# Kernel optimization log

Hardware: AMD Instinct MI355X
Metric: run time of the kernel (lower is better)

## Reference

```python
import jax, jax.numpy as jnp
import numpy as np

N_STEPS = 64          # sample['N']
G = 1.0               # sample['g'] (constant diffusion)
NUM_SAMPLES = 2       # num_samples_per_obs
W_SCALE = 0.05

# interpolant coefficients: alpha(s)=1-s, beta(s)=s, sigma(s)=1-s
# derivatives: alpha_dot=-1, beta_dot=1, sigma_dot=-1

def b_net(x, x0, s, W1, b1, W2, b2, W3, b3):
    # B_net(interpolant, current_state, s): MLP on concat([x, x0, s])
    sf = jnp.full(x.shape[:-1] + (1,), s, dtype=x.dtype)
    inp = jnp.concatenate([x, x0, sf], axis=-1)      # [B, 2*dim+1]
    h = jax.nn.relu(inp @ W1 + b1)
    h = jax.nn.relu(h @ W2 + b2)
    return h @ W3 + b3                                # [B, dim]


def setup_inputs() -> dict:
    key = jax.random.key(0)
    ks = jax.random.split(key, 4)
    num_obs, dim, hid = 65536, 64, 256
    X0 = jax.random.normal(ks[0], (num_obs, dim), dtype=jnp.float32)
    W1 = jax.random.normal(ks[1], (2 * dim + 1, hid), dtype=jnp.float32) * W_SCALE
    W2 = jax.random.normal(ks[2], (hid, hid), dtype=jnp.float32) * W_SCALE
    W3 = jax.random.normal(ks[3], (hid, dim), dtype=jnp.float32) * W_SCALE
    return {
        "X0": X0,
        "W1": W1, "b1": jnp.zeros((hid,), jnp.float32),
        "W2": W2, "b2": jnp.zeros((hid,), jnp.float32),
        "W3": W3, "b3": jnp.zeros((dim,), jnp.float32),
    }


def reference(X0, W1, b1, W2, b2, W3, b3):
    time = jnp.linspace(0.0, 1.0, N_STEPS + 1, dtype=X0.dtype)
    ds = jnp.asarray(1.0 / N_STEPS, X0.dtype)
    sqrt_ds = jnp.sqrt(ds)
    params = (W1, b1, W2, b2, W3, b3)

    def sample_one(key):
        k0, kloop = jax.random.split(key)
        # first Euler step: X = X0 + ds*B(X0,X0,0) + sigma(0)*sqrt(ds)*eta
        eta0 = jax.random.normal(k0, X0.shape, X0.dtype)
        X = X0 + ds * b_net(X0, X0, time[0], *params) + (1.0 - time[0]) * sqrt_ds * eta0

        def step(carry, n):
            X, key = carry
            key, kn = jax.random.split(key)
            s = time[n]
            al, ald = 1.0 - s, -1.0
            bt, btd = s, 1.0
            sg, sgd = 1.0 - s, -1.0
            drift_b = b_net(X, X0, s, *params)
            # score correction (self.score)
            c = btd * X + (bt * ald - btd * al) * X0
            A = 1.0 / (s * sg * (btd * sg - bt * sgd))
            score = A * (bt * drift_b - c)
            # adjusted drift: drift + 0.5*(g^2 - sigma^2)*score
            control = 0.5 * (G ** 2 - sg ** 2) * score
            eta = jax.random.normal(kn, X.shape, X.dtype)
            X = X + ds * (drift_b + control) + G * sqrt_ds * eta
            return (X, key), None

        (X, _), _ = jax.lax.scan(step, (X, kloop), jnp.arange(1, N_STEPS))
        return X

    keys = jax.random.split(jax.random.key(1), NUM_SAMPLES)
    samples = jax.vmap(sample_one)(keys)   # [num_samples, num_obs, dim]
    return samples
```

## Files before the change

### kernel.cpp

```cpp
#include <hip/hip_runtime.h>
#include <stdint.h>


#define PARTITIONABLE 1

namespace {

constexpr int   kObs    = 65536;
constexpr int   kDim    = 64;
constexpr int   kSteps  = 64;
constexpr float kDs     = 1.0f / 64.0f;
constexpr float kSqrtDs = 0.125f;

constexpr int kWeightBytes = 256 * 1024;
constexpr int kKeysOff     = kWeightBytes;
constexpr int kStabOff     = kKeysOff + 1024;

typedef _Float16 f16x8 __attribute__((ext_vector_type(8)));
typedef _Float16 f16x4 __attribute__((ext_vector_type(4)));
typedef float    f32x4 __attribute__((ext_vector_type(4)));

#define MFMA16(a, b, c) __builtin_amdgcn_mfma_f32_16x16x32_f16((a), (b), (c), 0, 0, 0)

__device__ __forceinline__ uint32_t rotl(uint32_t v, int r) {
  return (v << r) | (v >> (32 - r));
}

__device__ __forceinline__ void tf2x32(uint32_t k0, uint32_t k1,
                                       uint32_t& x0, uint32_t& x1) {
  uint32_t k2 = k0 ^ k1 ^ 0x1BD11BDAu;
  x0 += k0; x1 += k1;
  x0 += x1; x1 = rotl(x1, 13); x1 ^= x0;
  x0 += x1; x1 = rotl(x1, 15); x1 ^= x0;
  x0 += x1; x1 = rotl(x1, 26); x1 ^= x0;
  x0 += x1; x1 = rotl(x1,  6); x1 ^= x0;
  x0 += k1; x1 += k2 + 1u;
  x0 += x1; x1 = rotl(x1, 17); x1 ^= x0;
  x0 += x1; x1 = rotl(x1, 29); x1 ^= x0;
  x0 += x1; x1 = rotl(x1, 16); x1 ^= x0;
  x0 += x1; x1 = rotl(x1, 24); x1 ^= x0;
  x0 += k2; x1 += k0 + 2u;
  x0 += x1; x1 = rotl(x1, 13); x1 ^= x0;
  x0 += x1; x1 = rotl(x1, 15); x1 ^= x0;
  x0 += x1; x1 = rotl(x1, 26); x1 ^= x0;
  x0 += x1; x1 = rotl(x1,  6); x1 ^= x0;
  x0 += k0; x1 += k1 + 3u;
  x0 += x1; x1 = rotl(x1, 17); x1 ^= x0;
  x0 += x1; x1 = rotl(x1, 29); x1 ^= x0;
  x0 += x1; x1 = rotl(x1, 16); x1 ^= x0;
  x0 += x1; x1 = rotl(x1, 24); x1 ^= x0;
  x0 += k1; x1 += k2 + 4u;
  x0 += x1; x1 = rotl(x1, 13); x1 ^= x0;
  x0 += x1; x1 = rotl(x1, 15); x1 ^= x0;
  x0 += x1; x1 = rotl(x1, 26); x1 ^= x0;
  x0 += x1; x1 = rotl(x1,  6); x1 ^= x0;
  x0 += k2; x1 += k0 + 5u;
}

__device__ __forceinline__ void jax_split(uint32_t k0, uint32_t k1,
                                          uint32_t& a0, uint32_t& a1,
                                          uint32_t& b0, uint32_t& b1) {
#if PARTITIONABLE
  uint32_t x0 = 0u, x1 = 0u; tf2x32(k0, k1, x0, x1); a0 = x0; a1 = x1;
  uint32_t y0 = 0u, y1 = 1u; tf2x32(k0, k1, y0, y1); b0 = y0; b1 = y1;
#else
  uint32_t x0 = 0u, x1 = 2u; tf2x32(k0, k1, x0, x1);
  uint32_t y0 = 1u, y1 = 3u; tf2x32(k0, k1, y0, y1);
  a0 = x0; a1 = y0; b0 = x1; b1 = y1;
#endif
}

__device__ __forceinline__ uint32_t draw_bits(uint32_t k0, uint32_t k1, uint32_t i) {
#if PARTITIONABLE
  uint32_t x0 = 0u, x1 = i;
  tf2x32(k0, k1, x0, x1);
  return x0 ^ x1;
#else
  const uint32_t half = (uint32_t)kObs * kDim / 2;
  if (i < half) {
    uint32_t x0 = i, x1 = i + half; tf2x32(k0, k1, x0, x1); return x0;
  } else {
    uint32_t x0 = i - half, x1 = i; tf2x32(k0, k1, x0, x1); return x1;
  }
#endif
}

__device__ __forceinline__ float erfinv32(float x) {
  float w = -__logf(fmaf(-x, x, 1.0f));
  float p;
  if (w < 5.0f) {
    w = w - 2.5f;
    p =            2.81022636e-08f;
    p = fmaf(p, w, 3.43273939e-07f);
    p = fmaf(p, w, -3.5233877e-06f);
    p = fmaf(p, w, -4.39150654e-06f);
    p = fmaf(p, w, 0.00021858087f);
    p = fmaf(p, w, -0.00125372503f);
    p = fmaf(p, w, -0.00417768164f);
    p = fmaf(p, w, 0.246640727f);
    p = fmaf(p, w, 1.50140941f);
  } else {
    w = sqrtf(w) - 3.0f;
    p =            -0.000200214257f;
    p = fmaf(p, w, 0.000100950558f);
    p = fmaf(p, w, 0.00134934322f);
    p = fmaf(p, w, -0.00367342844f);
    p = fmaf(p, w, 0.00573950773f);
    p = fmaf(p, w, -0.0076224613f);
    p = fmaf(p, w, 0.00943887047f);
    p = fmaf(p, w, 1.00167406f);
    p = fmaf(p, w, 2.83297682f);
  }
  return p * x;
}

__device__ __forceinline__ float bits_to_normal(uint32_t bits) {
  const float lo = -0.99999994f;
  float f = __uint_as_float(0x3f800000u | (bits >> 9)) - 1.0f;
  float u = fmaxf(lo, fmaf(f, 2.0f, lo));
  return 1.41421356237f * erfinv32(u);
}

}

__global__ void prep_weights(const float* __restrict__ W1,
                             const float* __restrict__ W2,
                             const float* __restrict__ W3,
                             _Float16* __restrict__ ws) {
  const int G = blockIdx.x;
  const int t = threadIdx.x;

  if (G >= 256) {
    if (t < 2) {
      uint32_t* kout = (uint32_t*)((char*)ws + kKeysOff) + t * 128;
      uint32_t s0a, s0b, s1a, s1b;
      jax_split(0u, 1u, s0a, s0b, s1a, s1b);
      const uint32_t sk0 = t ? s1a : s0a;
      const uint32_t sk1 = t ? s1b : s0b;
      uint32_t kd0, kd1, kl0, kl1;
      jax_split(sk0, sk1, kd0, kd1, kl0, kl1);
      kout[0] = kd0; kout[1] = kd1;
      for (int n = 1; n < kSteps; ++n) {
        uint32_t na, nb, xa, xb;
        jax_split(kl0, kl1, na, nb, xa, xb);
        kl0 = na; kl1 = nb;
        kout[2 * n] = xa; kout[2 * n + 1] = xb;
      }
    }
    if (t < kSteps) {
      const float s  = (float)t * kDs;
      const float sg = 1.0f - s;
      f32x4 v;
      v[0] = s;
      v[1] = (t == 0) ? 0.0f : 1.0f / (s * sg);
      v[2] = 0.5f * (1.0f - sg * sg);
      v[3] = 0.0f;
      *(f32x4*)((char*)ws + kStabOff + t * 16) = v;
    }
    return;
  }

  const int lane = t >> 2;
  const int j0   = (t & 3) * 2;
  const int w    = G >> 5;
  const int T    = G & 31;
  const int lm   = lane & 15;
  const int kb   = (lane >> 4) << 3;

#pragma unroll
  for (int jj = 0; jj < 2; ++jj) {
    const int j = j0 + jj;
    float v;
    if (T < 8) {
      const int mt = T >> 2, kt = T & 3;
      const int col = w * 32 + mt * 16 + lm;
      const int k   = kt * 32 + kb + j;
      v = W1[k * 256 + col];
    } else if (T < 24) {
      const int u = T - 8;
      const int mt = u >> 3, kt = u & 7;
      const int col = w * 32 + mt * 16 + lm;
      const int k   = kt * 32 + kb + j;
      v = W2[k * 256 + col];
    } else {
      const int kt  = T - 24;
      const int col = (w >> 1) * 16 + lm;
      const int k   = kt * 32 + kb + j;
      v = W3[k * 64 + col];
    }
    ws[(size_t)G * 512 + lane * 8 + j] = (_Float16)v;
  }
}

__global__ __launch_bounds__(512, 2)
void sde_mfma(const float* __restrict__ X0g,
              const float* __restrict__ W1,
              const float* __restrict__ b1,
              const float* __restrict__ b2,
              const float* __restrict__ b3,
              const _Float16* __restrict__ ws,
              float* __restrict__ out) {
  __shared__ alignas(16) char  xAf [8 * 1024];
  __shared__ alignas(16) char  x0Af[8 * 1024];
  __shared__ alignas(16) char  h1f [32 * 1024];
  __shared__ alignas(16) char  h2f [32 * 1024];
  __shared__ alignas(16) float bb  [832];

  const int t    = threadIdx.x;
  const int w    = t >> 6;
  const int l    = t & 63;
  const int lq   = l >> 4;
  const int lm   = l & 15;
  const int samp = blockIdx.x >> 10;
  const int tile = blockIdx.x & 1023;
  const int r0   = tile * 64;
  const int mt3  = w >> 1;
  const int ntb  = (w & 1) * 2;
  const int d0   = mt3 * 16 + lq * 4;

  const int rb  = l * 16;
  const int lo1 = ((lq >> 1) * 16 + lm) * 16 + (lq & 1) * 8;
  const int kt3 = mt3 >> 1;
  const int ln3 = (((mt3 & 1) * 2 + (lq >> 1)) * 16 + lm) * 16 + (lq & 1) * 8;

  if (t < 256) {
    bb[t]       = b1[t];
    bb[256 + t] = W1[128 * 256 + t];
    bb[512 + t] = b2[t];
  } else if (t < 320) {
    bb[768 + (t - 256)] = b3[t - 256];
  }

  {
    const int li = t >> 3;
    const int ci = (t & 7) * 8;
    const float* p = X0g + (size_t)(r0 + li) * kDim + ci;
    const float4 a = *(const float4*)p;
    const float4 b = *(const float4*)(p + 4);
    f16x8 h;
    h[0] = (_Float16)a.x; h[1] = (_Float16)a.y;
    h[2] = (_Float16)a.z; h[3] = (_Float16)a.w;
    h[4] = (_Float16)b.x; h[5] = (_Float16)b.y;
    h[6] = (_Float16)b.z; h[7] = (_Float16)b.w;
    const int fa = ((ci >> 5) * 4 + (li >> 4)) * 1024 +
                   (((ci >> 3) & 3) * 16 + (li & 15)) * 16;
    *(f16x8*)(xAf  + fa) = h;
    *(f16x8*)(x0Af + fa) = h;
  }

  float xv[2][4];
  f32x4 x0q[2];
#pragma unroll
  for (int ni = 0; ni < 2; ++ni) {
    const int row = (ntb + ni) * 16 + lm;
    x0q[ni] = *(const f32x4*)(X0g + (size_t)(r0 + row) * kDim + d0);
#pragma unroll
    for (int q = 0; q < 4; ++q) xv[ni][q] = x0q[ni][q];
  }
  const uint32_t giA = (uint32_t)((r0 + ntb * 16 + lm) * kDim + d0);
  const uint32_t giB = giA + 16u * kDim;

  f16x8 wreg[32];
  {
    const char* pW = (const char*)ws + (size_t)w * 32768 + l * 16;
#pragma unroll
    for (int i = 0; i < 32; ++i)
      wreg[i] = *(const f16x8*)(pW + i * 1024);
  }

  const uint32_t* keys = (const uint32_t*)((const char*)ws + kKeysOff) + samp * 128;
  const f32x4*    stab = (const f32x4*)((const char*)ws + kStabOff);

  __syncthreads();

  for (int n = 0; n < kSteps; ++n) {
    const f32x4 st = stab[n];
    const float s = st[0], A = st[1], coef = st[2];
    const uint32_t ka = keys[2 * n], kbk = keys[2 * n + 1];

    float etaA[4];
#pragma unroll
    for (int q = 0; q < 4; ++q)
      etaA[q] = bits_to_normal(draw_bits(ka, kbk, giA + q));

#pragma unroll
    for (int nt = 0; nt < 4; ++nt) {
      f16x8 bf[4];
      bf[0] = *(const f16x8*)(xAf  + (0 * 4 + nt) * 1024 + rb);
      bf[1] = *(const f16x8*)(xAf  + (1 * 4 + nt) * 1024 + rb);
      bf[2] = *(const f16x8*)(x0Af + (0 * 4 + nt) * 1024 + rb);
      bf[3] = *(const f16x8*)(x0Af + (1 * 4 + nt) * 1024 + rb);
#pragma unroll
      for (int mt = 0; mt < 2; ++mt) {
        f32x4 c = {0.f, 0.f, 0.f, 0.f};
#pragma unroll
        for (int kt = 0; kt < 4; ++kt)
          c = MFMA16(wreg[mt * 4 + kt], bf[kt], c);
        const int nb = w * 32 + mt * 16 + lq * 4;
        const f32x4 bq = *(const f32x4*)&bb[nb];
        const f32x4 wq = *(const f32x4*)&bb[256 + nb];
        f16x4 o;
#pragma unroll
        for (int q = 0; q < 4; ++q)
          o[q] = (_Float16)fmaxf(c[q] + fmaf(s, wq[q], bq[q]), 0.f);
        *(f16x4*)(h1f + (w * 4 + nt) * 1024 + mt * 512 + lo1) = o;
      }
    }
    __syncthreads();

#pragma unroll
    for (int ntp = 0; ntp < 2; ++ntp) {
      f32x4 c[2][2];
#pragma unroll
      for (int mt = 0; mt < 2; ++mt)
#pragma unroll
        for (int ni = 0; ni < 2; ++ni)
          c[mt][ni] = (f32x4){0.f, 0.f, 0.f, 0.f};
#pragma unroll
      for (int half = 0; half < 2; ++half) {
        f16x8 bh[2][4];
#pragma unroll
        for (int ni = 0; ni < 2; ++ni)
#pragma unroll
          for (int k4 = 0; k4 < 4; ++k4)
            bh[ni][k4] = *(const f16x8*)
                (h1f + ((half * 4 + k4) * 4 + ntp * 2 + ni) * 1024 + rb);
#pragma unroll
        for (int mt = 0; mt < 2; ++mt)
#pragma unroll
          for (int k4 = 0; k4 < 4; ++k4) {
            const f16x8 aW = wreg[8 + mt * 8 + half * 4 + k4];
            c[mt][0] = MFMA16(aW, bh[0][k4], c[mt][0]);
            c[mt][1] = MFMA16(aW, bh[1][k4], c[mt][1]);
          }
      }
#pragma unroll
      for (int mt = 0; mt < 2; ++mt) {
        const int nb = w * 32 + mt * 16 + lq * 4;
        const f32x4 bq = *(const f32x4*)&bb[512 + nb];
#pragma unroll
        for (int ni = 0; ni < 2; ++ni) {
          f16x4 o;
#pragma unroll
          for (int q = 0; q < 4; ++q)
            o[q] = (_Float16)fmaxf(c[mt][ni][q] + bq[q], 0.f);
          *(f16x4*)(h2f + (w * 4 + ntp * 2 + ni) * 1024 + mt * 512 + lo1) = o;
        }
      }
    }

    float etaB[4];
#pragma unroll
    for (int q = 0; q < 4; ++q)
      etaB[q] = bits_to_normal(draw_bits(ka, kbk, giB + q));
    __syncthreads();

    const f32x4 b3q = *(const f32x4*)&bb[768 + d0];
#pragma unroll
    for (int ni = 0; ni < 2; ++ni) {
      f32x4 dA = {0.f, 0.f, 0.f, 0.f}, dB = {0.f, 0.f, 0.f, 0.f};
#pragma unroll
      for (int half = 0; half < 2; ++half) {
        f16x8 bh[4];
#pragma unroll
        for (int k4 = 0; k4 < 4; ++k4)
          bh[k4] = *(const f16x8*)
              (h2f + ((half * 4 + k4) * 4 + ntb + ni) * 1024 + rb);
        dA = MFMA16(wreg[24 + half * 4 + 0], bh[0], dA);
        dB = MFMA16(wreg[24 + half * 4 + 1], bh[1], dB);
        dA = MFMA16(wreg[24 + half * 4 + 2], bh[2], dA);
        dB = MFMA16(wreg[24 + half * 4 + 3], bh[3], dB);
      }
      f16x4 hx;
#pragma unroll
      for (int q = 0; q < 4; ++q) {
        const float ov    = dA[q] + dB[q] + b3q[q];
        const float eta   = ni ? etaB[q] : etaA[q];
        const float score = A * (s * ov - (xv[ni][q] - x0q[ni][q]));
        const float nx    = xv[ni][q] + kDs * (ov + coef * score) + kSqrtDs * eta;
        xv[ni][q] = nx;
        hx[q] = (_Float16)nx;
      }
      *(f16x4*)(xAf + (kt3 * 4 + ntb + ni) * 1024 + ln3) = hx;
    }
    __syncthreads();
  }

#pragma unroll
  for (int ni = 0; ni < 2; ++ni) {
    const int row = (ntb + ni) * 16 + lm;
    const size_t ob = (size_t)samp * ((size_t)kObs * kDim) +
                      (size_t)(r0 + row) * kDim + d0;
    f32x4 v;
#pragma unroll
    for (int q = 0; q < 4; ++q) v[q] = xv[ni][q];
    *(f32x4*)(out + ob) = v;
  }
}

extern "C" void kernel_launch(void* const* d_in, const int* in_sizes, int n_in,
                              void* d_out, int out_size, void* d_ws, size_t ws_size,
                              hipStream_t stream) {
  const float* X0 = (const float*)d_in[0];
  const float* W1 = (const float*)d_in[1];
  const float* b1 = (const float*)d_in[2];
  const float* W2 = (const float*)d_in[3];
  const float* b2 = (const float*)d_in[4];
  const float* W3 = (const float*)d_in[5];
  const float* b3 = (const float*)d_in[6];
  _Float16* ws = (_Float16*)d_ws;

  prep_weights<<<dim3(257), dim3(256), 0, stream>>>(W1, W2, W3, ws);
  sde_mfma<<<dim3(2048), dim3(512), 0, stream>>>(X0, W1, b1, b2, b3, ws,
                                                 (float*)d_out);
}
```

Measured before the change: 2.934 ms.

## Precompute loop-invariant X0 half of layer-1 and prefetch next-step noise

Layer 1's contribution from X0 never changes across steps, so it is computed once with MFMA before the loop, kept in registers as fp16, and added each step. Each step now runs half the layer-1 MFMAs and no longer needs the x0 shared buffer. Noise for the next step is generated in the middle of layer 2 so its ALU work can overlap with MFMA. The update folds ds*coef*A into one precomputed constant applied through fmas. The cost is extra registers for the fp16 precompute, plus rounding it to fp16, which changes accuracy slightly.

```diff
diff --git a/kernel.cpp b/kernel.cpp
--- a/kernel.cpp
+++ b/kernel.cpp
@@ -154,7 +154,7 @@
       v[0] = s;
       v[1] = (t == 0) ? 0.0f : 1.0f / (s * sg);
       v[2] = 0.5f * (1.0f - sg * sg);
-      v[3] = 0.0f;
+      v[3] = kDs * v[2] * v[1];
       *(f32x4*)((char*)ws + kStabOff + t * 16) = v;
     }
     return;
@@ -201,7 +201,6 @@
               const _Float16* __restrict__ ws,
               float* __restrict__ out) {
   __shared__ alignas(16) char  xAf [8 * 1024];
-  __shared__ alignas(16) char  x0Af[8 * 1024];
   __shared__ alignas(16) char  h1f [32 * 1024];
   __shared__ alignas(16) char  h2f [32 * 1024];
   __shared__ alignas(16) float bb  [832];
@@ -244,8 +243,8 @@
     h[6] = (_Float16)b.z; h[7] = (_Float16)b.w;
     const int fa = ((ci >> 5) * 4 + (li >> 4)) * 1024 +
                    (((ci >> 3) & 3) * 16 + (li & 15)) * 16;
-    *(f16x8*)(xAf  + fa) = h;
-    *(f16x8*)(x0Af + fa) = h;
+    *(f16x8*)(xAf + fa) = h;
+    *(f16x8*)(h1f + fa) = h;
   }
 
   float xv[2][4];
@@ -260,54 +259,81 @@
   const uint32_t giA = (uint32_t)((r0 + ntb * 16 + lm) * kDim + d0);
   const uint32_t giB = giA + 16u * kDim;
 
-  f16x8 wreg[32];
-  {
-    const char* pW = (const char*)ws + (size_t)w * 32768 + l * 16;
-#pragma unroll
-    for (int i = 0; i < 32; ++i)
-      wreg[i] = *(const f16x8*)(pW + i * 1024);
-  }
+  const char* pW = (const char*)ws + (size_t)w * 32768 + l * 16;
+  f16x8 wL1[2][2], wx0[2][2], wL2[16], wL3[8];
+#pragma unroll
+  for (int mt = 0; mt < 2; ++mt) {
+    wL1[mt][0] = *(const f16x8*)(pW + (mt * 4 + 0) * 1024);
+    wL1[mt][1] = *(const f16x8*)(pW + (mt * 4 + 1) * 1024);
+    wx0[mt][0] = *(const f16x8*)(pW + (mt * 4 + 2) * 1024);
+    wx0[mt][1] = *(const f16x8*)(pW + (mt * 4 + 3) * 1024);
+  }
+#pragma unroll
+  for (int i = 0; i < 16; ++i) wL2[i] = *(const f16x8*)(pW + (8 + i) * 1024);
+#pragma unroll
+  for (int i = 0; i < 8; ++i)  wL3[i] = *(const f16x8*)(pW + (24 + i) * 1024);
 
   const uint32_t* keys = (const uint32_t*)((const char*)ws + kKeysOff) + samp * 128;
   const f32x4*    stab = (const f32x4*)((const char*)ws + kStabOff);
 
   __syncthreads();
 
+  f16x4 pre[4][2];
+#pragma unroll
+  for (int nt = 0; nt < 4; ++nt) {
+    const f16x8 xf0 = *(const f16x8*)(h1f + (0 * 4 + nt) * 1024 + rb);
+    const f16x8 xf1 = *(const f16x8*)(h1f + (1 * 4 + nt) * 1024 + rb);
+#pragma unroll
+    for (int mt = 0; mt < 2; ++mt) {
+      f32x4 p = {0.f, 0.f, 0.f, 0.f};
+      p = MFMA16(wx0[mt][0], xf0, p);
+      p = MFMA16(wx0[mt][1], xf1, p);
+      f16x4 ph;
+#pragma unroll
+      for (int q = 0; q < 4; ++q) ph[q] = (_Float16)p[q];
+      pre[nt][mt] = ph;
+    }
+  }
+  __syncthreads();
+
+  float etaA[4], etaB[4];
+  {
+    const uint32_t ka = keys[0], kb0 = keys[1];
+#pragma unroll
+    for (int q = 0; q < 4; ++q) etaA[q] = bits_to_normal(draw_bits(ka, kb0, giA + q));
+#pragma unroll
+    for (int q = 0; q < 4; ++q) etaB[q] = bits_to_normal(draw_bits(ka, kb0, giB + q));
+  }
+
   for (int n = 0; n < kSteps; ++n) {
     const f32x4 st = stab[n];
-    const float s = st[0], A = st[1], coef = st[2];
-    const uint32_t ka = keys[2 * n], kbk = keys[2 * n + 1];
-
-    float etaA[4];
-#pragma unroll
-    for (int q = 0; q < 4; ++q)
-      etaA[q] = bits_to_normal(draw_bits(ka, kbk, giA + q));
+    const float s = st[0], P = st[3];
+    const int np = (n + 1 < kSteps) ? n + 1 : n;
+    const uint32_t kna = keys[2 * np], knb = keys[2 * np + 1];
 
 #pragma unroll
     for (int nt = 0; nt < 4; ++nt) {
-      f16x8 bf[4];
-      bf[0] = *(const f16x8*)(xAf  + (0 * 4 + nt) * 1024 + rb);
-      bf[1] = *(const f16x8*)(xAf  + (1 * 4 + nt) * 1024 + rb);
-      bf[2] = *(const f16x8*)(x0Af + (0 * 4 + nt) * 1024 + rb);
-      bf[3] = *(const f16x8*)(x0Af + (1 * 4 + nt) * 1024 + rb);
+      const f16x8 bf0 = *(const f16x8*)(xAf + (0 * 4 + nt) * 1024 + rb);
+      const f16x8 bf1 = *(const f16x8*)(xAf + (1 * 4 + nt) * 1024 + rb);
 #pragma unroll
       for (int mt = 0; mt < 2; ++mt) {
         f32x4 c = {0.f, 0.f, 0.f, 0.f};
-#pragma unroll
-        for (int kt = 0; kt < 4; ++kt)
-          c = MFMA16(wreg[mt * 4 + kt], bf[kt], c);
+        c = MFMA16(wL1[mt][0], bf0, c);
+        c = MFMA16(wL1[mt][1], bf1, c);
         const int nb = w * 32 + mt * 16 + lq * 4;
         const f32x4 bq = *(const f32x4*)&bb[nb];
         const f32x4 wq = *(const f32x4*)&bb[256 + nb];
+        const f16x4 ph = pre[nt][mt];
         f16x4 o;
 #pragma unroll
         for (int q = 0; q < 4; ++q)
-          o[q] = (_Float16)fmaxf(c[q] + fmaf(s, wq[q], bq[q]), 0.f);
+          o[q] = (_Float16)fmaxf(c[q] + (float)ph[q] + fmaf(s, wq[q], bq[q]), 0.f);
         *(f16x4*)(h1f + (w * 4 + nt) * 1024 + mt * 512 + lo1) = o;
       }
     }
     __syncthreads();
 
+    float enA[4], enB[4];
 #pragma unroll
     for (int ntp = 0; ntp < 2; ++ntp) {
       f32x4 c[2][2];
@@ -329,10 +355,19 @@
         for (int mt = 0; mt < 2; ++mt)
 #pragma unroll
           for (int k4 = 0; k4 < 4; ++k4) {
-            const f16x8 aW = wreg[8 + mt * 8 + half * 4 + k4];
+            const f16x8 aW = wL2[mt * 8 + half * 4 + k4];
             c[mt][0] = MFMA16(aW, bh[0][k4], c[mt][0]);
             c[mt][1] = MFMA16(aW, bh[1][k4], c[mt][1]);
           }
+      }
+      if (ntp == 0) {
+#pragma unroll
+        for (int q = 0; q < 4; ++q)
+          enA[q] = bits_to_normal(draw_bits(kna, knb, giA + q));
+      } else {
+#pragma unroll
+        for (int q = 0; q < 4; ++q)
+          enB[q] = bits_to_normal(draw_bits(kna, knb, giB + q));
       }
 #pragma unroll
       for (int mt = 0; mt < 2; ++mt) {
@@ -348,11 +383,6 @@
         }
       }
     }
-
-    float etaB[4];
-#pragma unroll
-    for (int q = 0; q < 4; ++q)
-      etaB[q] = bits_to_normal(draw_bits(ka, kbk, giB + q));
     __syncthreads();
 
     const f32x4 b3q = *(const f32x4*)&bb[768 + d0];
@@ -366,23 +396,27 @@
         for (int k4 = 0; k4 < 4; ++k4)
           bh[k4] = *(const f16x8*)
               (h2f + ((half * 4 + k4) * 4 + ntb + ni) * 1024 + rb);
-        dA = MFMA16(wreg[24 + half * 4 + 0], bh[0], dA);
-        dB = MFMA16(wreg[24 + half * 4 + 1], bh[1], dB);
-        dA = MFMA16(wreg[24 + half * 4 + 2], bh[2], dA);
-        dB = MFMA16(wreg[24 + half * 4 + 3], bh[3], dB);
+        dA = MFMA16(wL3[half * 4 + 0], bh[0], dA);
+        dB = MFMA16(wL3[half * 4 + 1], bh[1], dB);
+        dA = MFMA16(wL3[half * 4 + 2], bh[2], dA);
+        dB = MFMA16(wL3[half * 4 + 3], bh[3], dB);
       }
       f16x4 hx;
 #pragma unroll
       for (int q = 0; q < 4; ++q) {
-        const float ov    = dA[q] + dB[q] + b3q[q];
-        const float eta   = ni ? etaB[q] : etaA[q];
-        const float score = A * (s * ov - (xv[ni][q] - x0q[ni][q]));
-        const float nx    = xv[ni][q] + kDs * (ov + coef * score) + kSqrtDs * eta;
+        const float ov  = dA[q] + dB[q] + b3q[q];
+        const float eta = ni ? etaB[q] : etaA[q];
+        const float t1  = fmaf(s, ov, x0q[ni][q] - xv[ni][q]);
+        float nx = fmaf(kSqrtDs, eta, xv[ni][q]);
+        nx = fmaf(kDs, ov, nx);
+        nx = fmaf(P, t1, nx);
         xv[ni][q] = nx;
         hx[q] = (_Float16)nx;
       }
       *(f16x4*)(xAf + (kt3 * 4 + ntb + ni) * 1024 + ln3) = hx;
     }
+#pragma unroll
+    for (int q = 0; q < 4; ++q) { etaA[q] = enA[q]; etaB[q] = enB[q]; }
     __syncthreads();
   }
 
```

Result: faster. 2.798 ms (median of 2 runs) (-4.6%).
